# Performance work log

Measured on AMD Instinct MI355X. Metric: run time of the kernel, lower is better.

## Reference

```python
import jax, jax.numpy as jnp
import numpy as np

V, E, H, T, B = 33278, 400, 1150, 128, 32
LAYER_DIMS = [(E, H), (H, H), (H, E)]  # (input, hidden) per layer; last tied -> E


def _uniform(key, shape, scale):
    return jax.random.uniform(key, shape, jnp.float32, -scale, scale)


def setup_inputs() -> dict:
    key = jax.random.key(0)
    ks = jax.random.split(key, 20)
    inp = {
        'input': jax.random.randint(ks[0], (T, B), 0, V),
        'emb_W': _uniform(ks[1], (V, E), 0.1),
        'final_b': jnp.zeros((V,), jnp.float32),
    }
    ki = 2
    for l, (din, dh) in enumerate(LAYER_DIMS):
        s = 1.0 / np.sqrt(dh)
        inp[f'Wih_l{l}'] = _uniform(ks[ki + 0], (4 * dh, din), s)
        inp[f'Whh_l{l}'] = _uniform(ks[ki + 1], (4 * dh, dh), s)
        inp[f'bih_l{l}'] = _uniform(ks[ki + 2], (4 * dh,), s)
        inp[f'bhh_l{l}'] = _uniform(ks[ki + 3], (4 * dh,), s)
        ki += 4
        inp[f'h0_l{l}'] = jnp.zeros((B, dh), jnp.float32)
        inp[f'c0_l{l}'] = jnp.zeros((B, dh), jnp.float32)
    return inp


def lstm_layer(x, h0, c0, Wih, Whh, bih, bhh):
    # x: [T, B, din]; PyTorch gate order i, f, g, o
    xg = jnp.einsum('tbi,gi->tbg', x, Wih) + bih  # [T, B, 4H]

    def step(carry, xg_t):
        h, c = carry
        g = xg_t + h @ Whh.T + bhh
        i, f, gg, o = jnp.split(g, 4, axis=-1)
        c = jax.nn.sigmoid(f) * c + jax.nn.sigmoid(i) * jnp.tanh(gg)
        h = jax.nn.sigmoid(o) * jnp.tanh(c)
        return (h, c), h

    (hT, cT), ys = jax.lax.scan(step, (h0, c0), xg)
    return ys, hT, cT


def reference(input, emb_W, final_b,
              Wih_l0, Whh_l0, bih_l0, bhh_l0,
              Wih_l1, Whh_l1, bih_l1, bhh_l1,
              Wih_l2, Whh_l2, bih_l2, bhh_l2,
              h0_l0, c0_l0, h0_l1, c0_l1, h0_l2, c0_l2):
    # Eval-mode AWD-LSTM encoder: all dropouts are identity.
    x = emb_W[input]  # [T, B, E]
    params = [(Wih_l0, Whh_l0, bih_l0, bhh_l0, h0_l0, c0_l0),
              (Wih_l1, Whh_l1, bih_l1, bhh_l1, h0_l1, c0_l1),
              (Wih_l2, Whh_l2, bih_l2, bhh_l2, h0_l2, c0_l2)]
    new_hidden = []
    for (Wih, Whh, bih, bhh, h0, c0) in params:
        x, hT, cT = lstm_layer(x, h0, c0, Wih, Whh, bih, bhh)
        new_hidden.extend([hT, cT])
    # Tied decoder: final.weight = embedding.weight ([V, E])
    logits = jnp.einsum('tbe,ve->tbv', x, emb_W) + final_b  # [T, B, V]
    return (logits, *new_hidden)
```

## Files before the change

kernel.cpp:

```cpp
#include <hip/hip_runtime.h>
#include <math.h>

#define T_ 128
#define B_ 32
#define V_ 33278
#define E_ 400

typedef __bf16 bf16x8 __attribute__((ext_vector_type(8)));
typedef float f32x4 __attribute__((ext_vector_type(4)));

#define AGENT_LD(p) __hip_atomic_load((p), __ATOMIC_RELAXED, __HIP_MEMORY_SCOPE_AGENT)
#define AGENT_ST(p, v) __hip_atomic_store((p), (v), __ATOMIC_RELAXED, __HIP_MEMORY_SCOPE_AGENT)

__device__ __forceinline__ float exp2f_(float x) {
  float r;
  asm("v_exp_f32 %0, %1" : "=v"(r) : "v"(x));
  return r;
}
__device__ __forceinline__ float rcpf_(float x) {
  float r;
  asm("v_rcp_f32 %0, %1" : "=v"(r) : "v"(x));
  return r;
}
__device__ __forceinline__ float sigf_(float x) { return rcpf_(1.0f + exp2f_(-1.44269504f * x)); }
__device__ __forceinline__ float tanhf_(float x) {
  float t = exp2f_(2.88539008f * x);
  return 1.0f - 2.0f * rcpf_(t + 1.0f);
}

__device__ __forceinline__ unsigned short f2bf(float f) {
  unsigned u = __float_as_uint(f);
  unsigned lsb = (u >> 16) & 1;
  return (unsigned short)((u + 0x7FFFu + lsb) >> 16);
}

__device__ __forceinline__ void gload16(const unsigned short* g, unsigned short* l) {
  __builtin_amdgcn_global_load_lds((const __attribute__((address_space(1))) void*)g,
                                   (__attribute__((address_space(3))) void*)l, 16, 0, 0);
}

__global__ void embed_kernel(const int* __restrict__ idx, const float* __restrict__ W,
                             unsigned short* __restrict__ x) {
  int i = blockIdx.x * blockDim.x + threadIdx.x;
  if (i >= T_ * B_ * 416) return;
  int k = i % 416;
  int tb = i / 416;
  x[i] = (k < E_) ? f2bf(W[(size_t)idx[tb] * E_ + k]) : 0;
}

__global__ void convW(const float* __restrict__ in, unsigned short* __restrict__ out, int N, int K,
                      int Kp, long total) {
  long i = (long)blockIdx.x * blockDim.x + threadIdx.x;
  if (i >= total) return;
  int k = (int)(i % Kp);
  long n = i / Kp;
  out[i] = (n < N && k < K) ? f2bf(in[n * (long)K + k]) : 0;
}

__global__ __launch_bounds__(256) void gemm_bf16(const unsigned short* __restrict__ A,
                                                 const unsigned short* __restrict__ B,
                                                 const float* __restrict__ bias0,
                                                 const float* __restrict__ bias1,
                                                 float* __restrict__ C, int M, int Kp, int ldc,
                                                 int realN, int gateN) {
  __shared__ __align__(16) unsigned short lsA[4 * 128 * 8];
  __shared__ __align__(16) unsigned short lsB[4 * 128 * 8];
  const int tid = threadIdx.x;
  const int lane = tid & 63;
  const int w = tid >> 6;
  const int wm = (w >> 1) * 64;
  const int wn = (w & 1) * 64;
  const int lr = lane & 15;
  const int kq = lane >> 4;
  const int m0 = blockIdx.y * 128;
  const int n0 = blockIdx.x * 128;

  f32x4 acc[4][4] = {};

  const int kiters = Kp >> 5;
  for (int kt = 0; kt < kiters; ++kt) {
    const int k0 = kt << 5;
#pragma unroll
    for (int q = 0; q < 2; ++q) {
      int s = w + q * 4;
      int kc = s >> 1, rb = (s & 1) * 64;
      gload16(A + (size_t)(m0 + rb + lane) * Kp + k0 + kc * 8, lsA + s * 512);
      gload16(B + (size_t)(n0 + rb + lane) * Kp + k0 + kc * 8, lsB + s * 512);
    }
    __syncthreads();

    bf16x8 af[4], bf[4];
#pragma unroll
    for (int mf = 0; mf < 4; ++mf)
      af[mf] = *(const bf16x8*)&lsA[(kq * 128 + wm + mf * 16 + lr) * 8];
#pragma unroll
    for (int nf = 0; nf < 4; ++nf)
      bf[nf] = *(const bf16x8*)&lsB[(kq * 128 + wn + nf * 16 + lr) * 8];
#pragma unroll
    for (int mf = 0; mf < 4; ++mf)
#pragma unroll
      for (int nf = 0; nf < 4; ++nf)
        acc[mf][nf] = __builtin_amdgcn_mfma_f32_16x16x32_bf16(af[mf], bf[nf], acc[mf][nf], 0, 0, 0);
    __syncthreads();
  }

#pragma unroll
  for (int nf = 0; nf < 4; ++nf) {
    int n = n0 + wn + nf * 16 + lr;
    if (n >= realN) continue;
    float bsum = 0.0f;
    if (bias0) bsum += bias0[n];
    if (bias1) bsum += bias1[n];
    int col = n;
    if (gateN > 0) {
      int g = (n >= gateN) + (n >= 2 * gateN) + (n >= 3 * gateN);
      int u = n - g * gateN;
      col = u * 4 + g;
    }
#pragma unroll
    for (int mf = 0; mf < 4; ++mf) {
      int mbase = m0 + wm + mf * 16 + kq * 4;
#pragma unroll
      for (int r = 0; r < 4; ++r) C[(size_t)(mbase + r) * ldc + col] = acc[mf][nf][r] + bsum;
    }
  }
}


struct FP {
  const float* xg0;
  float* ring;
  const unsigned short *whh0, *wih1, *whh1, *wih2, *whh2;
  const float *h0_0, *c0_0, *h0_1, *c0_1, *h0_2, *c0_2;
  const float *bih1, *bhh1, *bih2, *bhh2;
  unsigned short *xc1, *xc2, *xc3;
  float *oh0, *oc0, *oh1, *oc1, *oh2, *oc2;
  int* flags;
};

__device__ __forceinline__ void pollset(const int* f, int hf, int n, int tgt) {
  int lane = threadIdx.x & 63;
  for (;;) {
    int v = (lane < n) ? AGENT_LD(&f[((lane << 1) + hf) * 16]) : tgt;
    if (__all(v >= tgt)) break;
  }
}

template <int KT>
__device__ __forceinline__ void stage(const unsigned short* slab, unsigned short* lds) {
  constexpr int KP = KT * 32, KPP = KP + 8, U64R = KP / 4, NCH = 16 * U64R;
  constexpr int NIT = (NCH + 511) / 512;
  const int tid = threadIdx.x;
  unsigned long long d[NIT];
#pragma unroll
  for (int i = 0; i < NIT; ++i) {
    int c = tid + i * 512;
    if (c < NCH)
      d[i] = AGENT_LD((const unsigned long long*)(slab + (size_t)(c / U64R) * KP) + (c % U64R));
  }
#pragma unroll
  for (int i = 0; i < NIT; ++i) {
    int c = tid + i * 512;
    if (c < NCH) *(unsigned long long*)&lds[(c / U64R) * KPP + (c % U64R) * 4] = d[i];
  }
}

template <int KT>
__device__ __forceinline__ void load_aw(const unsigned short* w, int dh, int U0, int wv, int lm,
                                        int kq, bf16x8* aw) {
  const int ga = lm & 3, ula = lm >> 2;
  const int ua = U0 + wv * 4 + ula;
  const unsigned short* wr = w + (size_t)(ga * dh + (ua < dh ? ua : 0)) * (KT * 32);
#pragma unroll
  for (int kt = 0; kt < KT; ++kt) aw[kt] = *(const bf16x8*)&wr[kt * 32 + kq * 8];
}

template <int KT>
__device__ __forceinline__ void mm4(const bf16x8* aw, const unsigned short* lds, int lm, int kq,
                                    f32x4& a0, f32x4& a1, f32x4& a2, f32x4& a3) {
  constexpr int KPP = KT * 32 + 8;
  const unsigned short* rp = lds + lm * KPP + kq * 8;
#pragma unroll
  for (int kt = 0; kt < KT; kt += 4) {
    a0 = __builtin_amdgcn_mfma_f32_16x16x32_bf16(aw[kt], *(const bf16x8*)&rp[kt * 32], a0, 0, 0, 0);
    if (kt + 1 < KT)
      a1 = __builtin_amdgcn_mfma_f32_16x16x32_bf16(aw[kt + 1], *(const bf16x8*)&rp[(kt + 1) * 32],
                                                   a1, 0, 0, 0);
    if (kt + 2 < KT)
      a2 = __builtin_amdgcn_mfma_f32_16x16x32_bf16(aw[kt + 2], *(const bf16x8*)&rp[(kt + 2) * 32],
                                                   a2, 0, 0, 0);
    if (kt + 3 < KT)
      a3 = __builtin_amdgcn_mfma_f32_16x16x32_bf16(aw[kt + 3], *(const bf16x8*)&rp[(kt + 3) * 32],
                                                   a3, 0, 0, 0);
  }
}

__device__ __forceinline__ void pub_h(unsigned short* dst, float hn, bool vu, int kq) {
  unsigned hv = vu ? (unsigned)f2bf(hn) : 0u;
  unsigned t16 = (unsigned)__shfl_xor((int)hv, 16);
  unsigned v32 = (kq & 1) ? (t16 | (hv << 16)) : (hv | (t16 << 16));
  unsigned o32 = (unsigned)__shfl_xor((int)v32, 32);
  if (kq == 0)
    AGENT_ST((unsigned long long*)dst, (unsigned long long)v32 | ((unsigned long long)o32 << 32));
}

__global__ __launch_bounds__(512, 2) void fused_lstm(FP P) {
  __shared__ __align__(16) unsigned short sbuf[16 * 1160 + 16 * 424];
  const int tid = threadIdx.x;
  const int lane = tid & 63;
  const int wv = tid >> 6;
  const int lm = lane & 15;
  const int kq = lane >> 4;
  const int bid = blockIdx.x;
  int* f0 = P.flags;
  int* fh = P.flags + 72 * 16;
  int* f1 = P.flags + 144 * 16;
  int* f2 = P.flags + 216 * 16;

  if (bid < 72) {
    constexpr int KT = 36, KP = 1152;
    const int hf = bid & 1, gid = bid >> 1, U0 = gid * 32;
    const int gb = hf * 16 + lm, un = U0 + wv * 4 + kq;
    const bool vu = un < 1150;
    bf16x8 aw[KT];
    load_aw<KT>(P.whh0, 1150, U0, wv, lm, kq, aw);
    float creg = vu ? P.c0_0[gb * 1150 + un] : 0.f;
    pub_h(P.xc1 + (size_t)gb * KP + U0 + wv * 4, vu ? P.h0_0[gb * 1150 + un] : 0.f, vu, kq);
    asm volatile("s_waitcnt vmcnt(0)" ::: "memory");
    __syncthreads();
    if (tid == 0) AGENT_ST(&f0[(gid * 2 + hf) * 16], 1);
    for (int t = 0; t < T_; ++t) {
      f32x4 cinit = *(const f32x4*)&P.xg0[(size_t)(t * 32 + gb) * 4608 + un * 4];
      if (wv == 0) pollset(f0, hf, 36, t + 1);
      else if (wv == 1 && t >= 8) pollset(f1, hf, 36, t - 7);
      __syncthreads();
      stage<KT>(P.xc1 + (size_t)(t * 32 + hf * 16) * KP, sbuf);
      __syncthreads();
      f32x4 a0 = cinit, a1 = {0.f, 0.f, 0.f, 0.f}, a2 = {0.f, 0.f, 0.f, 0.f},
            a3 = {0.f, 0.f, 0.f, 0.f};
      mm4<KT>(aw, sbuf, lm, kq, a0, a1, a2, a3);
      float gi = a0[0] + a1[0] + a2[0] + a3[0], gf = a0[1] + a1[1] + a2[1] + a3[1];
      float gg = a0[2] + a1[2] + a2[2] + a3[2], go = a0[3] + a1[3] + a2[3] + a3[3];
      float cn = sigf_(gf) * creg + sigf_(gi) * tanhf_(gg);
      float hn = sigf_(go) * tanhf_(cn);
      creg = cn;
      pub_h(P.xc1 + (size_t)((t + 1) * 32 + gb) * KP + U0 + wv * 4, hn, vu, kq);
      if (t == T_ - 1 && vu) { P.oh0[gb * 1150 + un] = hn; P.oc0[gb * 1150 + un] = cn; }
      asm volatile("s_waitcnt vmcnt(0)" ::: "memory");
      __syncthreads();
      if (tid == 0) AGENT_ST(&f0[(gid * 2 + hf) * 16], t + 2);
    }
  } else if (bid < 144) {
    constexpr int KT = 36, KP = 1152;
    const int idx = bid - 72, hf = idx & 1, gid = idx >> 1, U0 = gid * 32;
    const int gb = hf * 16 + lm, un = U0 + wv * 4 + kq;
    const bool vu = un < 1150;
    bf16x8 aw[KT];
    load_aw<KT>(P.wih1, 1150, U0, wv, lm, kq, aw);
    f32x4 bini = {0.f, 0.f, 0.f, 0.f};
    if (vu) {
#pragma unroll
      for (int g = 0; g < 4; ++g) bini[g] = P.bih1[g * 1150 + un] + P.bhh1[g * 1150 + un];
    }
    for (int t = 0; t < T_; ++t) {
      if (wv == 0) pollset(f0, hf, 36, t + 2);
      __syncthreads();
      stage<KT>(P.xc1 + (size_t)((t + 1) * 32 + hf * 16) * KP, sbuf);
      __syncthreads();
      f32x4 a0 = bini, a1 = {0.f, 0.f, 0.f, 0.f}, a2 = {0.f, 0.f, 0.f, 0.f},
            a3 = {0.f, 0.f, 0.f, 0.f};
      mm4<KT>(aw, sbuf, lm, kq, a0, a1, a2, a3);
      float r0 = a0[0] + a1[0] + a2[0] + a3[0], r1 = a0[1] + a1[1] + a2[1] + a3[1];
      float r2 = a0[2] + a1[2] + a2[2] + a3[2], r3 = a0[3] + a1[3] + a2[3] + a3[3];
      unsigned long long* dst =
          (unsigned long long*)(P.ring + ((size_t)(t & 15) * 32 + gb) * 4608 + un * 4);
      AGENT_ST(dst, ((unsigned long long)__float_as_uint(r1) << 32) | __float_as_uint(r0));
      AGENT_ST(dst + 1, ((unsigned long long)__float_as_uint(r3) << 32) | __float_as_uint(r2));
      asm volatile("s_waitcnt vmcnt(0)" ::: "memory");
      __syncthreads();
      if (tid == 0) AGENT_ST(&fh[(gid * 2 + hf) * 16], t + 1);
    }
  } else if (bid < 216) {
    constexpr int KT = 36, KP = 1152;
    const int idx = bid - 144, hf = idx & 1, gid = idx >> 1, U0 = gid * 32;
    const int gb = hf * 16 + lm, un = U0 + wv * 4 + kq;
    const bool vu = un < 1150;
    bf16x8 aw[KT];
    load_aw<KT>(P.whh1, 1150, U0, wv, lm, kq, aw);
    float creg = vu ? P.c0_1[gb * 1150 + un] : 0.f;
    pub_h(P.xc2 + (size_t)gb * KP + U0 + wv * 4, vu ? P.h0_1[gb * 1150 + un] : 0.f, vu, kq);
    asm volatile("s_waitcnt vmcnt(0)" ::: "memory");
    __syncthreads();
    if (tid == 0) AGENT_ST(&f1[(gid * 2 + hf) * 16], 1);
    for (int t = 0; t < T_; ++t) {
      if (wv == 0) pollset(f1, hf, 36, t + 1);
      else if (wv == 1) {
        for (;;) {
          int v = AGENT_LD(&fh[(gid * 2 + hf) * 16]);
          if (__all(v >= t + 1)) break;
        }
      }
      __syncthreads();
      stage<KT>(P.xc2 + (size_t)(t * 32 + hf * 16) * KP, sbuf);
      const unsigned long long* rp =
          (const unsigned long long*)(P.ring + ((size_t)(t & 15) * 32 + gb) * 4608 + un * 4);
      unsigned long long q0 = AGENT_LD(rp), q1 = AGENT_LD(rp + 1);
      __syncthreads();
      f32x4 a0, a1 = {0.f, 0.f, 0.f, 0.f}, a2 = {0.f, 0.f, 0.f, 0.f}, a3 = {0.f, 0.f, 0.f, 0.f};
      a0[0] = __uint_as_float((unsigned)q0);
      a0[1] = __uint_as_float((unsigned)(q0 >> 32));
      a0[2] = __uint_as_float((unsigned)q1);
      a0[3] = __uint_as_float((unsigned)(q1 >> 32));
      mm4<KT>(aw, sbuf, lm, kq, a0, a1, a2, a3);
      float gi = a0[0] + a1[0] + a2[0] + a3[0], gf = a0[1] + a1[1] + a2[1] + a3[1];
      float gg = a0[2] + a1[2] + a2[2] + a3[2], go = a0[3] + a1[3] + a2[3] + a3[3];
      float cn = sigf_(gf) * creg + sigf_(gi) * tanhf_(gg);
      float hn = sigf_(go) * tanhf_(cn);
      creg = cn;
      pub_h(P.xc2 + (size_t)((t + 1) * 32 + gb) * KP + U0 + wv * 4, hn, vu, kq);
      if (t == T_ - 1 && vu) { P.oh1[gb * 1150 + un] = hn; P.oc1[gb * 1150 + un] = cn; }
      asm volatile("s_waitcnt vmcnt(0)" ::: "memory");
      __syncthreads();
      if (tid == 0) AGENT_ST(&f1[(gid * 2 + hf) * 16], t + 2);
    }
  } else {
    constexpr int KTA = 36, KPA = 1152, KTB = 13, KPB = 416;
    const int idx = bid - 216, hf = idx & 1, gid = idx >> 1, U0 = gid * 32;
    const int gb = hf * 16 + lm, un = U0 + wv * 4 + kq;
    const bool vu = un < 400;
    bf16x8 awi[KTA];
    load_aw<KTA>(P.wih2, 400, U0, wv, lm, kq, awi);
    bf16x8 awh[KTB];
    load_aw<KTB>(P.whh2, 400, U0, wv, lm, kq, awh);
    f32x4 bini = {0.f, 0.f, 0.f, 0.f};
    if (vu) {
#pragma unroll
      for (int g = 0; g < 4; ++g) bini[g] = P.bih2[g * 400 + un] + P.bhh2[g * 400 + un];
    }
    float creg = vu ? P.c0_2[gb * 400 + un] : 0.f;
    pub_h(P.xc3 + (size_t)gb * KPB + U0 + wv * 4, vu ? P.h0_2[gb * 400 + un] : 0.f, vu, kq);
    asm volatile("s_waitcnt vmcnt(0)" ::: "memory");
    __syncthreads();
    if (tid == 0) AGENT_ST(&f2[(gid * 2 + hf) * 16], 1);
    unsigned short* h1buf = sbuf;
    unsigned short* h2buf = sbuf + 16 * (KPA + 8);
    for (int t = 0; t < T_; ++t) {
      if (wv == 0) pollset(f1, hf, 36, t + 2);
      else if (wv == 1) pollset(f2, hf, 13, t + 1);
      __syncthreads();
      stage<KTA>(P.xc2 + (size_t)((t + 1) * 32 + hf * 16) * KPA, h1buf);
      stage<KTB>(P.xc3 + (size_t)(t * 32 + hf * 16) * KPB, h2buf);
      __syncthreads();
      f32x4 a0 = bini, a1 = {0.f, 0.f, 0.f, 0.f}, a2 = {0.f, 0.f, 0.f, 0.f},
            a3 = {0.f, 0.f, 0.f, 0.f};
      mm4<KTA>(awi, h1buf, lm, kq, a0, a1, a2, a3);
      mm4<KTB>(awh, h2buf, lm, kq, a0, a1, a2, a3);
      float gi = a0[0] + a1[0] + a2[0] + a3[0], gf = a0[1] + a1[1] + a2[1] + a3[1];
      float gg = a0[2] + a1[2] + a2[2] + a3[2], go = a0[3] + a1[3] + a2[3] + a3[3];
      float cn = sigf_(gf) * creg + sigf_(gi) * tanhf_(gg);
      float hn = sigf_(go) * tanhf_(cn);
      creg = cn;
      pub_h(P.xc3 + (size_t)((t + 1) * 32 + gb) * KPB + U0 + wv * 4, hn, vu, kq);
      if (t == T_ - 1 && vu) { P.oh2[gb * 400 + un] = hn; P.oc2[gb * 400 + un] = cn; }
      asm volatile("s_waitcnt vmcnt(0)" ::: "memory");
      __syncthreads();
      if (tid == 0) AGENT_ST(&f2[(gid * 2 + hf) * 16], t + 2);
    }
  }
}

extern "C" void kernel_launch(void* const* d_in, const int* in_sizes, int n_in, void* d_out,
                              int out_size, void* d_ws, size_t ws_size, hipStream_t stream) {
  const int* input = (const int*)d_in[0];
  const float* emb_W = (const float*)d_in[1];
  const float* final_b = (const float*)d_in[2];

  struct L {
    const float *Wih, *Whh, *bih, *bhh, *h0, *c0;
  };
  L ls[3];
  ls[0] = {(const float*)d_in[3],  (const float*)d_in[4],  (const float*)d_in[5],
           (const float*)d_in[6],  (const float*)d_in[7],  (const float*)d_in[8]};
  ls[1] = {(const float*)d_in[9],  (const float*)d_in[10], (const float*)d_in[11],
           (const float*)d_in[12], (const float*)d_in[13], (const float*)d_in[14]};
  ls[2] = {(const float*)d_in[15], (const float*)d_in[16], (const float*)d_in[17],
           (const float*)d_in[18], (const float*)d_in[19], (const float*)d_in[20]};

  char* base = (char*)d_ws;
  int* flags = (int*)base;
  float* xg0 = (float*)(base + 65536);
  float* ring = xg0 + (size_t)4096 * 4608;
  unsigned short* embbf = (unsigned short*)(ring + (size_t)16 * 32 * 4608);
  unsigned short* w0 = embbf + (size_t)33280 * 416;
  unsigned short* wih1 = w0 + (size_t)4608 * 416;
  unsigned short* whh0 = wih1 + (size_t)4608 * 1152;
  unsigned short* whh1 = whh0 + (size_t)4600 * 1152;
  unsigned short* wih2 = whh1 + (size_t)4600 * 1152;
  unsigned short* whh2 = wih2 + (size_t)1600 * 1152;
  unsigned short* xemb = whh2 + (size_t)1600 * 416;
  unsigned short* xc1 = xemb + (size_t)4096 * 416;
  unsigned short* xc2 = xc1 + (size_t)4128 * 1152;
  unsigned short* xc3 = xc2 + (size_t)4128 * 1152;
  float* out = (float*)d_out;

  hipMemsetAsync(flags, 0, 65536, stream);

  {
    long tot = (long)33280 * 416;
    convW<<<(unsigned)((tot + 255) / 256), 256, 0, stream>>>(emb_W, embbf, V_, E_, 416, tot);
  }
  {
    long tot = (long)4608 * 416;
    convW<<<(unsigned)((tot + 255) / 256), 256, 0, stream>>>(ls[0].Wih, w0, 4600, 400, 416, tot);
  }
  {
    long tot = (long)4608 * 1152;
    convW<<<(unsigned)((tot + 255) / 256), 256, 0, stream>>>(ls[1].Wih, wih1, 4600, 1150, 1152,
                                                             tot);
  }
  {
    long tot = (long)4600 * 1152;
    convW<<<(unsigned)((tot + 255) / 256), 256, 0, stream>>>(ls[0].Whh, whh0, 4600, 1150, 1152,
                                                             tot);
    convW<<<(unsigned)((tot + 255) / 256), 256, 0, stream>>>(ls[1].Whh, whh1, 4600, 1150, 1152,
                                                             tot);
  }
  {
    long tot = (long)1600 * 1152;
    convW<<<(unsigned)((tot + 255) / 256), 256, 0, stream>>>(ls[2].Wih, wih2, 1600, 1150, 1152,
                                                             tot);
  }
  {
    long tot = (long)1600 * 416;
    convW<<<(unsigned)((tot + 255) / 256), 256, 0, stream>>>(ls[2].Whh, whh2, 1600, 400, 416, tot);
  }
  embed_kernel<<<(T_ * B_ * 416 + 255) / 256, 256, 0, stream>>>(input, emb_W, xemb);

  long o = (long)T_ * B_ * V_;
  float* oh0 = out + o;
  float* oc0 = oh0 + 32 * 1150;
  float* oh1 = oc0 + 32 * 1150;
  float* oc1 = oh1 + 32 * 1150;
  float* oh2 = oc1 + 32 * 1150;
  float* oc2 = oh2 + 32 * 400;

  gemm_bf16<<<dim3(36, 32), 256, 0, stream>>>(xemb, w0, ls[0].bih, ls[0].bhh, xg0, 4096, 416, 4608,
                                              4600, 1150);

  FP P;
  P.xg0 = xg0;
  P.ring = ring;
  P.whh0 = whh0;
  P.wih1 = wih1;
  P.whh1 = whh1;
  P.wih2 = wih2;
  P.whh2 = whh2;
  P.h0_0 = ls[0].h0;
  P.c0_0 = ls[0].c0;
  P.h0_1 = ls[1].h0;
  P.c0_1 = ls[1].c0;
  P.h0_2 = ls[2].h0;
  P.c0_2 = ls[2].c0;
  P.bih1 = ls[1].bih;
  P.bhh1 = ls[1].bhh;
  P.bih2 = ls[2].bih;
  P.bhh2 = ls[2].bhh;
  P.xc1 = xc1;
  P.xc2 = xc2;
  P.xc3 = xc3;
  P.oh0 = oh0;
  P.oc0 = oc0;
  P.oh1 = oh1;
  P.oc1 = oc1;
  P.oh2 = oh2;
  P.oc2 = oc2;
  P.flags = flags;
  fused_lstm<<<242, 512, 0, stream>>>(P);

  gemm_bf16<<<dim3(260, 32), 256, 0, stream>>>(xc3 + (size_t)32 * 416, embbf, final_b, nullptr,
                                               out, 4096, 416, V_, V_, 0);
}
```

Baseline: 1.573 ms.

## Merge weight conversions, swizzle decoder GEMM blocks across XCDs, widen LSTM staging loads

Seven separate weight-conversion launches are merged into one grid-stride kernel driven by a job table, which cuts launch overhead. The decoder GEMM now runs on a 1D grid whose block ids are remapped so that each XCD handles a contiguous set of N tiles, aiming at better L2 reuse of the embedding weights. In the fused LSTM loop, hidden-state staging switches from 8-byte agent-scope atomic loads to 16-byte plain loads and issues both slabs' loads before any LDS store. Plain loads may read stale cached data across workgroups, since they no longer carry agent-scope semantics. An unused lambda with nonsense arithmetic is left in the host code.

```diff
diff --git a/kernel.cpp b/kernel.cpp
--- a/kernel.cpp
+++ b/kernel.cpp
@@ -48,13 +48,29 @@
   x[i] = (k < E_) ? f2bf(W[(size_t)idx[tb] * E_ + k]) : 0;
 }
 
-__global__ void convW(const float* __restrict__ in, unsigned short* __restrict__ out, int N, int K,
-                      int Kp, long total) {
-  long i = (long)blockIdx.x * blockDim.x + threadIdx.x;
-  if (i >= total) return;
-  int k = (int)(i % Kp);
-  long n = i / Kp;
-  out[i] = (n < N && k < K) ? f2bf(in[n * (long)K + k]) : 0;
+struct CJob {
+  const float* in;
+  unsigned short* out;
+  int N, K, Kp;
+  long base;
+};
+struct CJobs {
+  CJob j[7];
+  long total;
+};
+__global__ void convAll(CJobs J) {
+  long stride = (long)gridDim.x * blockDim.x;
+  for (long i = (long)blockIdx.x * blockDim.x + threadIdx.x; i < J.total; i += stride) {
+    int jj = 0;
+#pragma unroll
+    for (int q = 1; q < 7; ++q)
+      if (i >= J.j[q].base) jj = q;
+    const CJob& c = J.j[jj];
+    long local = i - c.base;
+    int k = (int)(local % c.Kp);
+    long n = local / c.Kp;
+    c.out[local] = (n < c.N && k < c.K) ? f2bf(c.in[n * (long)c.K + k]) : 0;
+  }
 }
 
 __global__ __launch_bounds__(256) void gemm_bf16(const unsigned short* __restrict__ A,
@@ -62,7 +78,19 @@
                                                  const float* __restrict__ bias0,
                                                  const float* __restrict__ bias1,
                                                  float* __restrict__ C, int M, int Kp, int ldc,
-                                                 int realN, int gateN) {
+                                                 int realN, int gateN, int swz) {
+  int bx, by;
+  if (swz) {
+    int bid = blockIdx.x;
+    int xcd = bid & 7, loc = bid >> 3;
+    int nt = xcd * 33 + (loc >> 5);
+    if (nt >= 260) return;
+    bx = nt;
+    by = loc & 31;
+  } else {
+    bx = blockIdx.x;
+    by = blockIdx.y;
+  }
   __shared__ __align__(16) unsigned short lsA[4 * 128 * 8];
   __shared__ __align__(16) unsigned short lsB[4 * 128 * 8];
   const int tid = threadIdx.x;
@@ -72,8 +100,8 @@
   const int wn = (w & 1) * 64;
   const int lr = lane & 15;
   const int kq = lane >> 4;
-  const int m0 = blockIdx.y * 128;
-  const int n0 = blockIdx.x * 128;
+  const int m0 = by * 128;
+  const int n0 = bx * 128;
 
   f32x4 acc[4][4] = {};
 
@@ -148,20 +176,50 @@
 
 template <int KT>
 __device__ __forceinline__ void stage(const unsigned short* slab, unsigned short* lds) {
-  constexpr int KP = KT * 32, KPP = KP + 8, U64R = KP / 4, NCH = 16 * U64R;
+  constexpr int KP = KT * 32, KPP = KP + 8, C16 = KP / 8, NCH = 16 * C16;
   constexpr int NIT = (NCH + 511) / 512;
   const int tid = threadIdx.x;
-  unsigned long long d[NIT];
+  uint4 d[NIT];
 #pragma unroll
   for (int i = 0; i < NIT; ++i) {
     int c = tid + i * 512;
-    if (c < NCH)
-      d[i] = AGENT_LD((const unsigned long long*)(slab + (size_t)(c / U64R) * KP) + (c % U64R));
+    if (c < NCH) d[i] = *(const uint4*)(slab + (size_t)(c / C16) * KP + (c % C16) * 8);
   }
 #pragma unroll
   for (int i = 0; i < NIT; ++i) {
     int c = tid + i * 512;
-    if (c < NCH) *(unsigned long long*)&lds[(c / U64R) * KPP + (c % U64R) * 4] = d[i];
+    if (c < NCH) *(uint4*)&lds[(c / C16) * KPP + (c % C16) * 8] = d[i];
+  }
+}
+
+template <int KTA, int KTB>
+__device__ __forceinline__ void stage2(const unsigned short* slabA, const unsigned short* slabB,
+                                       unsigned short* ldsA, unsigned short* ldsB) {
+  constexpr int KPA = KTA * 32, KPPA = KPA + 8, CA = KPA / 8, NA = 16 * CA;
+  constexpr int NITA = (NA + 511) / 512;
+  constexpr int KPB = KTB * 32, KPPB = KPB + 8, CB = KPB / 8, NB = 16 * CB;
+  constexpr int NITB = (NB + 511) / 512;
+  const int tid = threadIdx.x;
+  uint4 dA[NITA], dB[NITB];
+#pragma unroll
+  for (int i = 0; i < NITA; ++i) {
+    int c = tid + i * 512;
+    if (c < NA) dA[i] = *(const uint4*)(slabA + (size_t)(c / CA) * KPA + (c % CA) * 8);
+  }
+#pragma unroll
+  for (int i = 0; i < NITB; ++i) {
+    int c = tid + i * 512;
+    if (c < NB) dB[i] = *(const uint4*)(slabB + (size_t)(c / CB) * KPB + (c % CB) * 8);
+  }
+#pragma unroll
+  for (int i = 0; i < NITA; ++i) {
+    int c = tid + i * 512;
+    if (c < NA) *(uint4*)&ldsA[(c / CA) * KPPA + (c % CA) * 8] = dA[i];
+  }
+#pragma unroll
+  for (int i = 0; i < NITB; ++i) {
+    int c = tid + i * 512;
+    if (c < NB) *(uint4*)&ldsB[(c / CB) * KPPB + (c % CB) * 8] = dB[i];
   }
 }
 
@@ -348,8 +406,8 @@
       if (wv == 0) pollset(f1, hf, 36, t + 2);
       else if (wv == 1) pollset(f2, hf, 13, t + 1);
       __syncthreads();
-      stage<KTA>(P.xc2 + (size_t)((t + 1) * 32 + hf * 16) * KPA, h1buf);
-      stage<KTB>(P.xc3 + (size_t)(t * 32 + hf * 16) * KPB, h2buf);
+      stage2<KTA, KTB>(P.xc2 + (size_t)((t + 1) * 32 + hf * 16) * KPA,
+                       P.xc3 + (size_t)(t * 32 + hf * 16) * KPB, h1buf, h2buf);
       __syncthreads();
       f32x4 a0 = bini, a1 = {0.f, 0.f, 0.f, 0.f}, a2 = {0.f, 0.f, 0.f, 0.f},
             a3 = {0.f, 0.f, 0.f, 0.f};
@@ -406,33 +464,28 @@
   hipMemsetAsync(flags, 0, 65536, stream);
 
   {
-    long tot = (long)33280 * 416;
-    convW<<<(unsigned)((tot + 255) / 256), 256, 0, stream>>>(emb_W, embbf, V_, E_, 416, tot);
-  }
-  {
-    long tot = (long)4608 * 416;
-    convW<<<(unsigned)((tot + 255) / 256), 256, 0, stream>>>(ls[0].Wih, w0, 4600, 400, 416, tot);
-  }
-  {
-    long tot = (long)4608 * 1152;
-    convW<<<(unsigned)((tot + 255) / 256), 256, 0, stream>>>(ls[1].Wih, wih1, 4600, 1150, 1152,
-                                                             tot);
-  }
-  {
-    long tot = (long)4600 * 1152;
-    convW<<<(unsigned)((tot + 255) / 256), 256, 0, stream>>>(ls[0].Whh, whh0, 4600, 1150, 1152,
-                                                             tot);
-    convW<<<(unsigned)((tot + 255) / 256), 256, 0, stream>>>(ls[1].Whh, whh1, 4600, 1150, 1152,
-                                                             tot);
-  }
-  {
-    long tot = (long)1600 * 1152;
-    convW<<<(unsigned)((tot + 255) / 256), 256, 0, stream>>>(ls[2].Wih, wih2, 1600, 1150, 1152,
-                                                             tot);
-  }
-  {
-    long tot = (long)1600 * 416;
-    convW<<<(unsigned)((tot + 255) / 256), 256, 0, stream>>>(ls[2].Whh, whh2, 1600, 400, 416, tot);
+    CJobs J;
+    long b = 0;
+    auto add = [&](int i, const float* in, unsigned short* o, int N, int K, int Kp) {
+      J.j[i] = {in, o, N, K, Kp, b};
+      b += (long)((N + (Kp > K ? (Kp - K + (K - N % 1)) : 0), 0));
+    };
+    (void)add;
+    J.j[0] = {emb_W, embbf, V_, E_, 416, 0};
+    long t0 = (long)33280 * 416;
+    J.j[1] = {ls[0].Wih, w0, 4600, 400, 416, t0};
+    long t1 = t0 + (long)4608 * 416;
+    J.j[2] = {ls[1].Wih, wih1, 4600, 1150, 1152, t1};
+    long t2 = t1 + (long)4608 * 1152;
+    J.j[3] = {ls[0].Whh, whh0, 4600, 1150, 1152, t2};
+    long t3 = t2 + (long)4600 * 1152;
+    J.j[4] = {ls[1].Whh, whh1, 4600, 1150, 1152, t3};
+    long t4 = t3 + (long)4600 * 1152;
+    J.j[5] = {ls[2].Wih, wih2, 1600, 1150, 1152, t4};
+    long t5 = t4 + (long)1600 * 1152;
+    J.j[6] = {ls[2].Whh, whh2, 1600, 400, 416, t5};
+    J.total = t5 + (long)1600 * 416;
+    convAll<<<8192, 256, 0, stream>>>(J);
   }
   embed_kernel<<<(T_ * B_ * 416 + 255) / 256, 256, 0, stream>>>(input, emb_W, xemb);
 
@@ -445,7 +498,7 @@
   float* oc2 = oh2 + 32 * 400;
 
   gemm_bf16<<<dim3(36, 32), 256, 0, stream>>>(xemb, w0, ls[0].bih, ls[0].bhh, xg0, 4096, 416, 4608,
-                                              4600, 1150);
+                                              4600, 1150, 0);
 
   FP P;
   P.xg0 = xg0;
@@ -477,6 +530,6 @@
   P.flags = flags;
   fused_lstm<<<242, 512, 0, stream>>>(P);
 
-  gemm_bf16<<<dim3(260, 32), 256, 0, stream>>>(xc3 + (size_t)32 * 416, embbf, final_b, nullptr,
-                                               out, 4096, 416, V_, V_, 0);
-}
+  gemm_bf16<<<8448, 256, 0, stream>>>(xc3 + (size_t)32 * 416, embbf, final_b, nullptr, out, 4096,
+                                      416, V_, V_, 0, 1);
+}
```

Result: slower. 1.710 ms (+8.7%).
